# Optimization experiments

Hardware: AMD Instinct MI355X
Metric: run time of the kernel (lower is better)

## Reference

```python
import jax, jax.numpy as jnp
import numpy as np

B, C, H, W = 2, 320, 48, 48
HEADS, DIM_HEAD, NUM_FILTERS = 8, 64, 32
INNER = HEADS * DIM_HEAD  # 512
LN_EPS = 1e-05


def setup_inputs() -> dict:
    key = jax.random.key(0)
    ks = jax.random.split(key, 8)
    w = 0.02
    return {
        "hidden_states": jax.random.normal(ks[0], (B, C, H, W), jnp.float32),
        "encoder_hidden_states": jax.random.normal(ks[1], (B, C, H, W), jnp.float32),
        "Wq": jax.random.normal(ks[2], (C, INNER), jnp.float32) * w,
        "Wk": jax.random.normal(ks[3], (C, INNER), jnp.float32) * w,
        "Wv": jax.random.normal(ks[4], (C, INNER), jnp.float32) * w,
        "Wo": jax.random.normal(ks[5], (INNER, C), jnp.float32) * w,
        "bo": jnp.zeros((C,), jnp.float32),
        "ln_gamma": jnp.ones((C,), jnp.float32),
        "ln_beta": jnp.zeros((C,), jnp.float32),
        "ex_filters": jax.random.normal(ks[6], (NUM_FILTERS, INNER), jnp.float32),
        "dist_filters": jax.random.normal(ks[7], (NUM_FILTERS, INNER), jnp.float32),
        "scale": jnp.ones((1,), jnp.float32),  # learnable scale shadows dim_head**-0.5
    }


def _split_heads(t, heads):
    b, s, d = t.shape
    return t.reshape(b, s, heads, d // heads).transpose(0, 2, 1, 3)  # [b,h,s,dh]


def reference(hidden_states, encoder_hidden_states, Wq, Wk, Wv, Wo, bo,
              ln_gamma, ln_beta, ex_filters, dist_filters, scale):
    b, c, h, w = hidden_states.shape
    _, _, rh, rw = encoder_hidden_states.shape
    residual = hidden_states
    s = scale[0]

    hs = hidden_states.transpose(0, 2, 3, 1).reshape(b, h * w, c)        # [b, q, C]
    ehs = encoder_hidden_states.transpose(0, 2, 3, 1).reshape(b, rh * rw, c)

    # LayerNorm on encoder states
    mu = ehs.mean(-1, keepdims=True)
    var = jnp.mean((ehs - mu) ** 2, axis=-1, keepdims=True)
    ehs = (ehs - mu) * jax.lax.rsqrt(var + LN_EPS) * ln_gamma + ln_beta

    q = _split_heads(hs @ Wq, HEADS)    # [b,h,q,dh]
    k = _split_heads(ehs @ Wk, HEADS)   # [b,h,kv,dh]
    v = _split_heads(ehs @ Wv, HEADS)   # [b,h,kv,dh]
    ef = _split_heads(jnp.broadcast_to(ex_filters[None], (b,) + ex_filters.shape), HEADS)   # [b,h,F,dh]
    df = _split_heads(jnp.broadcast_to(dist_filters[None], (b,) + dist_filters.shape), HEADS)

    # spatial attention: softmax over kv positions
    spatial = jax.nn.softmax(jnp.einsum('bhfd,bhkd->bhfk', ef, k) * s, axis=-1)   # [b,h,F,kv]
    # channel attention: softmax over the filter axis (torch dim=1 of [B*h, F, q])
    channel = jax.nn.softmax(jnp.einsum('bhfd,bhqd->bhfq', df, q) * s, axis=2)    # [b,h,F,q]

    attn = jnp.einsum('bhfq,bhfk->bhqk', channel, spatial)                        # [b,h,q,kv]
    out = jnp.einsum('bhqk,bhkd->bhqd', attn, v)                                  # [b,h,q,dh]

    out = out.transpose(0, 2, 1, 3).reshape(b, h * w, INNER)
    out = out @ Wo + bo
    out = out.reshape(b, h, w, c).transpose(0, 3, 1, 2)
    return out + residual * s
```

## Files before the change

kernel.cpp:

```cpp
#include <hip/hip_runtime.h>
#include <math.h>

#define Bc 2
#define Cc 320
#define Pc 2304
#define HEADSc 8
#define DHc 64
#define INNERc 512
#define Fc 32
#define LN_EPS 1e-5f
#define CHUNKS 18
#define CHUNK_P 128

typedef __attribute__((ext_vector_type(8))) short bf16x8;
typedef __attribute__((ext_vector_type(4))) float f32x4;

static __device__ __forceinline__ ushort f2bf(float x) {
  uint u = __builtin_bit_cast(uint, x);
  u = (u + 0x7fffu + ((u >> 16) & 1u)) >> 16;
  return (ushort)u;
}

static __device__ __forceinline__ void gload16(const ushort* g, ushort* l) {
  __builtin_amdgcn_global_load_lds(
      (const __attribute__((address_space(1))) uint*)g,
      (__attribute__((address_space(3))) uint*)l, 16, 0, 0);
}

static __device__ void transpose_tile(const float* __restrict__ src,
                                      ushort* __restrict__ dst, int R, int C,
                                      int r0, int c0, int tid,
                                      float (*t)[65]) {
#pragma unroll
  for (int it = 0; it < 4; ++it) {
    int lin = it * 256 + tid;
    int rr = lin >> 4, c4 = lin & 15;
    float4 v = *(const float4*)(&src[(size_t)(r0 + rr) * C + c0 + c4 * 4]);
    t[rr][c4 * 4 + 0] = v.x; t[rr][c4 * 4 + 1] = v.y;
    t[rr][c4 * 4 + 2] = v.z; t[rr][c4 * 4 + 3] = v.w;
  }
  __syncthreads();
#pragma unroll
  for (int it = 0; it < 2; ++it) {
    int lin = it * 256 + tid;
    int cc = lin >> 3, r8 = lin & 7;
    ushort tmp[8];
#pragma unroll
    for (int j = 0; j < 8; ++j) tmp[j] = f2bf(t[r8 * 8 + j][cc]);
    *(uint4*)(&dst[(size_t)(c0 + cc) * R + r0 + r8 * 8]) = *(const uint4*)tmp;
  }
}

__global__ __launch_bounds__(256) void prep_all_kernel(
    const float* __restrict__ hs, const float* __restrict__ ehs,
    const float* __restrict__ gamma, const float* __restrict__ beta,
    const float* __restrict__ Wv, const float* __restrict__ Wo,
    const float* __restrict__ exf, const float* __restrict__ Wk,
    const float* __restrict__ dif, const float* __restrict__ Wq,
    ushort* __restrict__ hsT, ushort* __restrict__ ehsT,
    ushort* __restrict__ WvT, ushort* __restrict__ WoT,
    ushort* __restrict__ Gk, ushort* __restrict__ Gq) {
  __shared__ float smem[6448];
  int idx = blockIdx.x, tid = threadIdx.x;

  if (idx < 144) {
    int pt = idx % 36, z = idx / 36;
    int b = z & 1, which = z >> 1;
    int pos0 = pt * 64;
    const float* src = (which ? ehs : hs) + (size_t)b * Cc * Pc;
    ushort* dst = (which ? ehsT : hsT) + (size_t)b * Pc * Cc;
    float* t = smem;
    float* s1 = smem + 4160;
    float* s2 = smem + 4416;
    float* lmean = smem + 4672;
    float* lrstd = smem + 4736;
    int lane = tid & 63, g = tid >> 6;
    if (which) {
      const float* base = src + pos0 + lane;
      float sum = 0.f, sq = 0.f;
      for (int c = g * 80; c < g * 80 + 80; ++c) {
        float x = base[(size_t)c * Pc];
        sum += x; sq += x * x;
      }
      s1[g * 64 + lane] = sum; s2[g * 64 + lane] = sq;
      __syncthreads();
      if (tid < 64) {
        float ts = s1[tid] + s1[64 + tid] + s1[128 + tid] + s1[192 + tid];
        float tq = s2[tid] + s2[64 + tid] + s2[128 + tid] + s2[192 + tid];
        float mean = ts / (float)Cc;
        float var = tq / (float)Cc - mean * mean;
        lmean[tid] = mean;
        lrstd[tid] = rsqrtf(var + LN_EPS);
      }
      __syncthreads();
    }
    for (int ct = 0; ct < 5; ++ct) {
      int r0 = ct * 64;
#pragma unroll
      for (int it = 0; it < 4; ++it) {
        int lin = it * 256 + tid;
        int rr = lin >> 4, c4 = lin & 15;
        float4 v = *(const float4*)(&src[(size_t)(r0 + rr) * Pc + pos0 + c4 * 4]);
        t[rr * 65 + c4 * 4 + 0] = v.x; t[rr * 65 + c4 * 4 + 1] = v.y;
        t[rr * 65 + c4 * 4 + 2] = v.z; t[rr * 65 + c4 * 4 + 3] = v.w;
      }
      __syncthreads();
#pragma unroll
      for (int it = 0; it < 2; ++it) {
        int lin = it * 256 + tid;
        int cc = lin >> 3, r8 = lin & 7;
        float m_ = which ? lmean[cc] : 0.f, rs_ = which ? lrstd[cc] : 1.f;
        ushort tmp[8];
#pragma unroll
        for (int j = 0; j < 8; ++j) {
          int ch = r8 * 8 + j;
          float x = t[ch * 65 + cc];
          float val = which ? (x - m_) * rs_ * gamma[r0 + ch] + beta[r0 + ch] : x;
          tmp[j] = f2bf(val);
        }
        *(uint4*)(&dst[(size_t)(pos0 + cc) * Cc + r0 + r8 * 8]) =
            *(const uint4*)tmp;
      }
      __syncthreads();
    }
  } else {
    int idx2 = idx - 144;
    if (idx2 < 40) {
      transpose_tile(Wv, WvT, Cc, INNERc, (idx2 / 8) * 64, (idx2 % 8) * 64,
                     tid, (float(*)[65])smem);
    } else if (idx2 < 80) {
      int i = idx2 - 40;
      transpose_tile(Wo, WoT, INNERc, Cc, (i / 5) * 64, (i % 5) * 64, tid,
                     (float(*)[65])smem);
    } else {
      int i = idx2 - 80;
      int c0 = (i % 5) * 64, h = (i / 5) % 8, zz = i / 40;
      const float* filt = zz ? dif : exf;
      const float* W = zz ? Wq : Wk;
      ushort* G = zz ? Gq : Gk;
      float (*ef)[66] = (float(*)[66])smem;
      float (*wk)[65] = (float(*)[65])(smem + 32 * 66);
      for (int l = tid; l < Fc * DHc; l += 256) {
        int f = l >> 6, d = l & 63;
        ef[f][d] = filt[(size_t)f * INNERc + h * 64 + d];
      }
      for (int l = tid; l < 64 * DHc; l += 256) {
        int cc = l >> 6, d = l & 63;
        wk[cc][d] = W[(size_t)(c0 + cc) * INNERc + h * 64 + d];
      }
      __syncthreads();
      int f = tid >> 3, cbase = tid & 7;
      float acc[8] = {};
#pragma unroll
      for (int d4 = 0; d4 < DHc; d4 += 4) {
        float4 a = *(const float4*)(&ef[f][d4]);
#pragma unroll
        for (int j = 0; j < 8; ++j) {
          float4 b = *(const float4*)(&wk[cbase + j * 8][d4]);
          acc[j] += a.x * b.x + a.y * b.y + a.z * b.z + a.w * b.w;
        }
      }
#pragma unroll
      for (int j = 0; j < 8; ++j)
        G[(size_t)(h * Fc + f) * Cc + c0 + cbase + j * 8] = f2bf(acc[j]);
    }
  }
}

__global__ __launch_bounds__(256) void spatial_kernel(
    const ushort* __restrict__ Gk, const ushort* __restrict__ ehsT,
    const ushort* __restrict__ WvT, const float* __restrict__ scale_p,
    float* __restrict__ svp, float* __restrict__ mj, float* __restrict__ lj) {
  int c = blockIdx.x, h = blockIdx.y, b = blockIdx.z;
  int tid = threadIdx.x, lane = tid & 63, wv = tid >> 6;
  int l15 = lane & 15, kq = lane >> 4;
  int pos0 = c * CHUNK_P;
  int bh = b * HEADSc + h;
  float s = scale_p[0];

  __shared__ alignas(16) ushort As[96 * 64];
  __shared__ alignas(16) ushort Bs[128 * 64];
  __shared__ float Sq[32 * 132];
  __shared__ alignas(16) ushort P[32 * 136];
  __shared__ alignas(16) ushort Vs[64 * 136];

  const ushort* Av = WvT + (size_t)(h * 64) * Cc;
  const ushort* Ag = Gk + (size_t)(h * Fc) * Cc;
  const ushort* Bb = ehsT + ((size_t)b * Pc + pos0) * Cc;

  f32x4 acc[6][2] = {};
  for (int k0 = 0; k0 < Cc; k0 += 64) {
#pragma unroll
    for (int it = 0; it < 3; ++it) {
      int lin = it * 256 + tid;
      int row = lin >> 3, p = lin & 7;
      int lc = p ^ (row & 7);
      const ushort* sp = (row < 64) ? (Av + (size_t)row * Cc + k0 + lc * 8)
                                    : (Ag + (size_t)(row - 64) * Cc + k0 + lc * 8);
      gload16(sp, &As[lin * 8]);
    }
#pragma unroll
    for (int it = 0; it < 4; ++it) {
      int lin = it * 256 + tid;
      int row = lin >> 3, p = lin & 7;
      int lc = p ^ (row & 7);
      gload16(Bb + (size_t)row * Cc + k0 + lc * 8, &Bs[lin * 8]);
    }
    __syncthreads();
#pragma unroll
    for (int ss = 0; ss < 2; ++ss) {
      bf16x8 af[6], bfr[2];
#pragma unroll
      for (int mt = 0; mt < 6; ++mt) {
        int m = mt * 16 + l15;
        int p = (ss * 4 + kq) ^ (m & 7);
        af[mt] = *(const bf16x8*)(&As[m * 64 + p * 8]);
      }
#pragma unroll
      for (int nt = 0; nt < 2; ++nt) {
        int n = wv * 32 + nt * 16 + l15;
        int p = (ss * 4 + kq) ^ (n & 7);
        bfr[nt] = *(const bf16x8*)(&Bs[n * 64 + p * 8]);
      }
#pragma unroll
      for (int mt = 0; mt < 6; ++mt)
#pragma unroll
        for (int nt = 0; nt < 2; ++nt)
          acc[mt][nt] = __builtin_amdgcn_mfma_f32_16x16x32_bf16(
              af[mt], bfr[nt], acc[mt][nt], 0, 0, 0);
    }
    __syncthreads();
  }
#pragma unroll
  for (int mt = 0; mt < 6; ++mt)
#pragma unroll
    for (int nt = 0; nt < 2; ++nt) {
      int col = wv * 32 + nt * 16 + l15;
#pragma unroll
      for (int r = 0; r < 4; ++r) {
        int row = mt * 16 + kq * 4 + r;
        if (mt < 4) Vs[row * 136 + col] = f2bf(acc[mt][nt][r]);
        else Sq[(row - 64) * 132 + col] = acc[mt][nt][r];
      }
    }
  __syncthreads();

  {
    int row = tid >> 3, sub = tid & 7;
    float vals[16];
    float m_ = -1e30f;
#pragma unroll
    for (int i = 0; i < 16; ++i) {
      vals[i] = s * Sq[row * 132 + sub * 16 + i];
      m_ = fmaxf(m_, vals[i]);
    }
    m_ = fmaxf(m_, __shfl_xor(m_, 1));
    m_ = fmaxf(m_, __shfl_xor(m_, 2));
    m_ = fmaxf(m_, __shfl_xor(m_, 4));
    float l_ = 0.f;
#pragma unroll
    for (int i = 0; i < 16; i += 2) {
      float e0 = __expf(vals[i] - m_);
      float e1 = __expf(vals[i + 1] - m_);
      l_ += e0 + e1;
      uint pk = (uint)f2bf(e0) | ((uint)f2bf(e1) << 16);
      *(uint*)(&P[row * 136 + sub * 16 + i]) = pk;
    }
    l_ += __shfl_xor(l_, 1);
    l_ += __shfl_xor(l_, 2);
    l_ += __shfl_xor(l_, 4);
    if (sub == 0) {
      mj[((size_t)c * 16 + bh) * Fc + row] = m_;
      lj[((size_t)c * 16 + bh) * Fc + row] = l_;
    }
  }
  __syncthreads();

  f32x4 acc2[2] = {};
#pragma unroll
  for (int ss = 0; ss < 4; ++ss) {
    bf16x8 af[2];
#pragma unroll
    for (int mt = 0; mt < 2; ++mt)
      af[mt] = *(const bf16x8*)(&P[(mt * 16 + l15) * 136 + ss * 32 + kq * 8]);
    bf16x8 bfr = *(const bf16x8*)(&Vs[(wv * 16 + l15) * 136 + ss * 32 + kq * 8]);
#pragma unroll
    for (int mt = 0; mt < 2; ++mt)
      acc2[mt] = __builtin_amdgcn_mfma_f32_16x16x32_bf16(af[mt], bfr, acc2[mt],
                                                         0, 0, 0);
  }
  float* op = svp + ((size_t)c * 16 + bh) * (Fc * DHc);
#pragma unroll
  for (int mt = 0; mt < 2; ++mt)
#pragma unroll
    for (int r = 0; r < 4; ++r)
      op[(mt * 16 + kq * 4 + r) * DHc + wv * 16 + l15] = acc2[mt][r];
}

__global__ __launch_bounds__(256) void sv_reduce_kernel(
    const float* __restrict__ svp, const float* __restrict__ mj,
    const float* __restrict__ lj, ushort* __restrict__ svT) {
  int idx = blockIdx.x * 256 + threadIdx.x;
  int d = idx & 63, fr = idx >> 6;
  int bh = fr >> 5, f = fr & 31;
  float m = -1e30f;
#pragma unroll
  for (int c = 0; c < CHUNKS; ++c)
    m = fmaxf(m, mj[((size_t)c * 16 + bh) * Fc + f]);
  float osum = 0.f, lsum = 0.f;
#pragma unroll
  for (int c = 0; c < CHUNKS; ++c) {
    float w = __expf(mj[((size_t)c * 16 + bh) * Fc + f] - m);
    osum += w * svp[((size_t)c * 16 + bh) * (Fc * DHc) + f * DHc + d];
    lsum += w * lj[((size_t)c * 16 + bh) * Fc + f];
  }
  svT[((size_t)bh * DHc + d) * Fc + f] = f2bf(osum / lsum);
}

__global__ __launch_bounds__(256) void channel_kernel(
    const ushort* __restrict__ Gq, const ushort* __restrict__ hsT,
    const ushort* __restrict__ svT, const float* __restrict__ scale_p,
    ushort* __restrict__ OAT) {
  int pb = blockIdx.x, hp = blockIdx.y, b = blockIdx.z;
  int pos0 = pb * 64;
  int tid = threadIdx.x, lane = tid & 63, wv = tid >> 6;
  int l15 = lane & 15, kq = lane >> 4;
  float s = scale_p[0];

  __shared__ alignas(16) ushort Aq[2 * 32 * 64];
  __shared__ alignas(16) ushort Bs[64 * 64];
  __shared__ float SO[64 * 68];
  __shared__ alignas(16) ushort Pt[64 * 40];
  __shared__ alignas(16) ushort svs[64 * 40];
  __shared__ float red[4 * 64];

  f32x4 acc[2][2] = {};
  const ushort* Bb = hsT + ((size_t)b * Pc + pos0) * Cc;
  for (int k0 = 0; k0 < Cc; k0 += 64) {
#pragma unroll
    for (int it = 0; it < 2; ++it) {
      int lin = it * 256 + tid;
      int hh = lin >> 8, row = (lin >> 3) & 31, p = lin & 7;
      int lc = p ^ (row & 7);
      gload16(Gq + (size_t)((hp * 2 + hh) * Fc + row) * Cc + k0 + lc * 8,
              &Aq[lin * 8]);
    }
#pragma unroll
    for (int it = 0; it < 2; ++it) {
      int lin = it * 256 + tid;
      int row = lin >> 3, p = lin & 7;
      int lc = p ^ (row & 7);
      gload16(Bb + (size_t)row * Cc + k0 + lc * 8, &Bs[lin * 8]);
    }
    __syncthreads();
#pragma unroll
    for (int ss = 0; ss < 2; ++ss) {
      int n = wv * 16 + l15;
      int pb_ = (ss * 4 + kq) ^ (n & 7);
      bf16x8 bfr = *(const bf16x8*)(&Bs[n * 64 + pb_ * 8]);
#pragma unroll
      for (int hh = 0; hh < 2; ++hh)
#pragma unroll
        for (int mt = 0; mt < 2; ++mt) {
          int m = mt * 16 + l15;
          int pa = (ss * 4 + kq) ^ (m & 7);
          bf16x8 af = *(const bf16x8*)(&Aq[hh * 2048 + m * 64 + pa * 8]);
          acc[hh][mt] = __builtin_amdgcn_mfma_f32_16x16x32_bf16(
              af, bfr, acc[hh][mt], 0, 0, 0);
        }
    }
    __syncthreads();
  }

  for (int hh = 0; hh < 2; ++hh) {
    int h = hp * 2 + hh;
#pragma unroll
    for (int mt = 0; mt < 2; ++mt)
#pragma unroll
      for (int r = 0; r < 4; ++r)
        SO[(mt * 16 + kq * 4 + r) * 68 + wv * 16 + l15] = acc[hh][mt][r];
    {
      int rr = tid >> 2, p = tid & 3;
      *(uint4*)(&svs[rr * 40 + p * 8]) = *(const uint4*)(
          svT + ((size_t)(b * HEADSc + h) * DHc + rr) * Fc + p * 8);
    }
    __syncthreads();
    {
      int pos = tid & 63, g = tid >> 6;
      float v8[8];
      float pm = -1e30f;
#pragma unroll
      for (int i = 0; i < 8; ++i) {
        v8[i] = s * SO[(g * 8 + i) * 68 + pos];
        pm = fmaxf(pm, v8[i]);
      }
      red[g * 64 + pos] = pm;
      __syncthreads();
      float m_ = fmaxf(fmaxf(red[pos], red[64 + pos]),
                       fmaxf(red[128 + pos], red[192 + pos]));
      __syncthreads();
      float ps = 0.f;
#pragma unroll
      for (int i = 0; i < 8; ++i) {
        v8[i] = __expf(v8[i] - m_);
        ps += v8[i];
      }
      red[g * 64 + pos] = ps;
      __syncthreads();
      float inv = 1.f / (red[pos] + red[64 + pos] + red[128 + pos] +
                         red[192 + pos]);
#pragma unroll
      for (int i = 0; i < 8; i += 2) {
        uint pk = (uint)f2bf(v8[i] * inv) | ((uint)f2bf(v8[i + 1] * inv) << 16);
        *(uint*)(&Pt[pos * 40 + g * 8 + i]) = pk;
      }
    }
    __syncthreads();
    {
      bf16x8 b_ = *(const bf16x8*)(&svs[(wv * 16 + l15) * 40 + kq * 8]);
      f32x4 acc3[4];
#pragma unroll
      for (int mt = 0; mt < 4; ++mt) {
        bf16x8 a_ = *(const bf16x8*)(&Pt[(mt * 16 + l15) * 40 + kq * 8]);
        f32x4 z = {0.f, 0.f, 0.f, 0.f};
        acc3[mt] = __builtin_amdgcn_mfma_f32_16x16x32_bf16(a_, b_, z, 0, 0, 0);
      }
#pragma unroll
      for (int mt = 0; mt < 4; ++mt)
#pragma unroll
        for (int r = 0; r < 4; ++r)
          SO[(mt * 16 + kq * 4 + r) * 68 + wv * 16 + l15] = acc3[mt][r];
    }
    __syncthreads();
#pragma unroll
    for (int it = 0; it < 2; ++it) {
      int lin = it * 256 + tid;
      int p = lin >> 3, c8 = lin & 7;
      ushort tmp[8];
#pragma unroll
      for (int j = 0; j < 8; ++j) tmp[j] = f2bf(SO[p * 68 + c8 * 8 + j]);
      *(uint4*)(&OAT[((size_t)b * Pc + pos0 + p) * INNERc + h * 64 + c8 * 8]) =
          *(const uint4*)tmp;
    }
    __syncthreads();
  }
}

__global__ __launch_bounds__(256) void gemm_mfma_kernel(
    const ushort* __restrict__ A, const ushort* __restrict__ Bt,
    float* __restrict__ Out, int K, int Mdim,
    const float* __restrict__ bias, const float* __restrict__ res,
    const float* __restrict__ scale_p) {
  int b = blockIdx.z;
  int n0 = blockIdx.x * 128, m0 = blockIdx.y * 64;
  int tid = threadIdx.x, lane = tid & 63, wv = tid >> 6;
  int l15 = lane & 15, kq = lane >> 4;
  __shared__ alignas(16) ushort As[64 * 64];
  __shared__ alignas(16) ushort Bs[128 * 64];
  const ushort* Ab = A + (size_t)m0 * K;
  const ushort* Bb = Bt + ((size_t)b * Pc + n0) * K;

  f32x4 acc[4][2] = {};
  for (int k0 = 0; k0 < K; k0 += 64) {
#pragma unroll
    for (int it = 0; it < 2; ++it) {
      int lin = it * 256 + tid;
      int row = lin >> 3, p = lin & 7;
      int lc = p ^ (row & 7);
      gload16(Ab + (size_t)row * K + k0 + lc * 8, &As[lin * 8]);
    }
#pragma unroll
    for (int it = 0; it < 4; ++it) {
      int lin = it * 256 + tid;
      int row = lin >> 3, p = lin & 7;
      int lc = p ^ (row & 7);
      gload16(Bb + (size_t)row * K + k0 + lc * 8, &Bs[lin * 8]);
    }
    __syncthreads();
#pragma unroll
    for (int ss = 0; ss < 2; ++ss) {
      bf16x8 af[4], bfr[2];
#pragma unroll
      for (int mt = 0; mt < 4; ++mt) {
        int m = mt * 16 + l15;
        int p = (ss * 4 + kq) ^ (m & 7);
        af[mt] = *(const bf16x8*)(&As[m * 64 + p * 8]);
      }
#pragma unroll
      for (int nt = 0; nt < 2; ++nt) {
        int n = wv * 32 + nt * 16 + l15;
        int p = (ss * 4 + kq) ^ (n & 7);
        bfr[nt] = *(const bf16x8*)(&Bs[n * 64 + p * 8]);
      }
#pragma unroll
      for (int mt = 0; mt < 4; ++mt)
#pragma unroll
        for (int nt = 0; nt < 2; ++nt)
          acc[mt][nt] = __builtin_amdgcn_mfma_f32_16x16x32_bf16(
              af[mt], bfr[nt], acc[mt][nt], 0, 0, 0);
    }
    __syncthreads();
  }
  float s = scale_p[0];
  float* Ob = Out + ((size_t)b * Mdim + m0) * Pc + n0;
  const float* rb = res + ((size_t)b * Mdim + m0) * Pc + n0;
#pragma unroll
  for (int mt = 0; mt < 4; ++mt)
#pragma unroll
    for (int nt = 0; nt < 2; ++nt) {
      int ncol = wv * 32 + nt * 16 + l15;
#pragma unroll
      for (int r = 0; r < 4; ++r) {
        int m = mt * 16 + kq * 4 + r;
        Ob[(size_t)m * Pc + ncol] =
            acc[mt][nt][r] + bias[m0 + m] + s * rb[(size_t)m * Pc + ncol];
      }
    }
}

extern "C" void kernel_launch(void* const* d_in, const int* in_sizes, int n_in,
                              void* d_out, int out_size, void* d_ws, size_t ws_size,
                              hipStream_t stream) {
  const float* hs    = (const float*)d_in[0];
  const float* ehs   = (const float*)d_in[1];
  const float* Wq    = (const float*)d_in[2];
  const float* Wk    = (const float*)d_in[3];
  const float* Wv    = (const float*)d_in[4];
  const float* Wo    = (const float*)d_in[5];
  const float* bo    = (const float*)d_in[6];
  const float* gamma = (const float*)d_in[7];
  const float* beta  = (const float*)d_in[8];
  const float* exf   = (const float*)d_in[9];
  const float* dif   = (const float*)d_in[10];
  const float* scale = (const float*)d_in[11];
  float* out = (float*)d_out;

  float* ws = (float*)d_ws;
  float* svp = ws;
  float* mj  = svp + 589824;
  float* lj  = mj + 9216;
  ushort* hsT  = (ushort*)(lj + 9216);
  ushort* ehsT = hsT + 1474560;
  ushort* WvT  = ehsT + 1474560;
  ushort* WoT  = WvT + 163840;
  ushort* Gk   = WoT + 163840;
  ushort* Gq   = Gk + 81920;
  ushort* svT  = Gq + 81920;
  ushort* OAT  = svT + 32768;

  prep_all_kernel<<<dim3(304), dim3(256), 0, stream>>>(
      hs, ehs, gamma, beta, Wv, Wo, exf, Wk, dif, Wq,
      hsT, ehsT, WvT, WoT, Gk, Gq);
  spatial_kernel<<<dim3(CHUNKS, HEADSc, Bc), dim3(256), 0, stream>>>(
      Gk, ehsT, WvT, scale, svp, mj, lj);
  sv_reduce_kernel<<<dim3(128), dim3(256), 0, stream>>>(svp, mj, lj, svT);
  channel_kernel<<<dim3(Pc / 64, HEADSc / 2, Bc), dim3(256), 0, stream>>>(
      Gq, hsT, svT, scale, OAT);
  gemm_mfma_kernel<<<dim3(Pc / 128, Cc / 64, Bc), dim3(256), 0, stream>>>(
      WoT, OAT, out, INNERc, Cc, bo, hs, scale);
}
```

Before: 136.1 us.

## Merge spatial and channel stages into one launch, fuse PV into output GEMM

```diff
diff --git a/kernel.cpp b/kernel.cpp
--- a/kernel.cpp
+++ b/kernel.cpp
@@ -59,9 +59,11 @@
     const float* __restrict__ dif, const float* __restrict__ Wq,
     ushort* __restrict__ hsT, ushort* __restrict__ ehsT,
     ushort* __restrict__ WvT, ushort* __restrict__ WoT,
-    ushort* __restrict__ Gk, ushort* __restrict__ Gq) {
+    ushort* __restrict__ Gk, ushort* __restrict__ Gq,
+    uint* __restrict__ cnt) {
   __shared__ float smem[6448];
   int idx = blockIdx.x, tid = threadIdx.x;
+  if (idx == 0 && tid < 16) cnt[tid] = 0;
 
   if (idx < 144) {
     int pt = idx % 36, z = idx / 36;
@@ -167,54 +169,351 @@
   }
 }
 
-__global__ __launch_bounds__(256) void spatial_kernel(
+__global__ __launch_bounds__(256) void mid_kernel(
     const ushort* __restrict__ Gk, const ushort* __restrict__ ehsT,
-    const ushort* __restrict__ WvT, const float* __restrict__ scale_p,
-    float* __restrict__ svp, float* __restrict__ mj, float* __restrict__ lj) {
-  int c = blockIdx.x, h = blockIdx.y, b = blockIdx.z;
+    const ushort* __restrict__ WvT, const ushort* __restrict__ Gq,
+    const ushort* __restrict__ hsT, const float* __restrict__ scale_p,
+    float* __restrict__ svp, float* __restrict__ mj, float* __restrict__ lj,
+    uint* __restrict__ cnt, ushort* __restrict__ svT,
+    ushort* __restrict__ Pn) {
+  __shared__ alignas(16) char smem[71680];
+  __shared__ int lastflag;
+  int tid = threadIdx.x;
+  int typ = (int)blockIdx.x & 1, sidx = (int)blockIdx.x >> 1;
+  int lane = tid & 63, wv = tid >> 6;
+  int l15 = lane & 15, kq = lane >> 4;
+  float s = scale_p[0];
+
+  if (typ == 0) {
+    int c = sidx % CHUNKS, h = (sidx / CHUNKS) & 7, b = sidx / (CHUNKS * 8);
+    int pos0 = c * CHUNK_P;
+    int bh = b * HEADSc + h;
+    ushort* As = (ushort*)smem;
+    ushort* Bs = (ushort*)(smem + 12288);
+    float* Sq = (float*)(smem + 28672);
+    ushort* P = (ushort*)(smem + 45568);
+    ushort* Vs = (ushort*)(smem + 54272);
+
+    const ushort* Av = WvT + (size_t)(h * 64) * Cc;
+    const ushort* Ag = Gk + (size_t)(h * Fc) * Cc;
+    const ushort* Bb = ehsT + ((size_t)b * Pc + pos0) * Cc;
+
+    f32x4 acc[6][2] = {};
+    for (int k0 = 0; k0 < Cc; k0 += 64) {
+#pragma unroll
+      for (int it = 0; it < 3; ++it) {
+        int lin = it * 256 + tid;
+        int row = lin >> 3, p = lin & 7;
+        int lc = p ^ (row & 7);
+        const ushort* sp = (row < 64)
+                               ? (Av + (size_t)row * Cc + k0 + lc * 8)
+                               : (Ag + (size_t)(row - 64) * Cc + k0 + lc * 8);
+        gload16(sp, &As[lin * 8]);
+      }
+#pragma unroll
+      for (int it = 0; it < 4; ++it) {
+        int lin = it * 256 + tid;
+        int row = lin >> 3, p = lin & 7;
+        int lc = p ^ (row & 7);
+        gload16(Bb + (size_t)row * Cc + k0 + lc * 8, &Bs[lin * 8]);
+      }
+      __syncthreads();
+#pragma unroll
+      for (int ss = 0; ss < 2; ++ss) {
+        bf16x8 af[6], bfr[2];
+#pragma unroll
+        for (int mt = 0; mt < 6; ++mt) {
+          int m = mt * 16 + l15;
+          int p = (ss * 4 + kq) ^ (m & 7);
+          af[mt] = *(const bf16x8*)(&As[m * 64 + p * 8]);
+        }
+#pragma unroll
+        for (int nt = 0; nt < 2; ++nt) {
+          int n = wv * 32 + nt * 16 + l15;
+          int p = (ss * 4 + kq) ^ (n & 7);
+          bfr[nt] = *(const bf16x8*)(&Bs[n * 64 + p * 8]);
+        }
+#pragma unroll
+        for (int mt = 0; mt < 6; ++mt)
+#pragma unroll
+          for (int nt = 0; nt < 2; ++nt)
+            acc[mt][nt] = __builtin_amdgcn_mfma_f32_16x16x32_bf16(
+                af[mt], bfr[nt], acc[mt][nt], 0, 0, 0);
+      }
+      __syncthreads();
+    }
+#pragma unroll
+    for (int mt = 0; mt < 6; ++mt)
+#pragma unroll
+      for (int nt = 0; nt < 2; ++nt) {
+        int col = wv * 32 + nt * 16 + l15;
+#pragma unroll
+        for (int r = 0; r < 4; ++r) {
+          int row = mt * 16 + kq * 4 + r;
+          if (mt < 4) Vs[row * 136 + col] = f2bf(acc[mt][nt][r]);
+          else Sq[(row - 64) * 132 + col] = acc[mt][nt][r];
+        }
+      }
+    __syncthreads();
+
+    {
+      int row = tid >> 3, sub = tid & 7;
+      float vals[16];
+      float m_ = -1e30f;
+#pragma unroll
+      for (int i = 0; i < 16; ++i) {
+        vals[i] = s * Sq[row * 132 + sub * 16 + i];
+        m_ = fmaxf(m_, vals[i]);
+      }
+      m_ = fmaxf(m_, __shfl_xor(m_, 1));
+      m_ = fmaxf(m_, __shfl_xor(m_, 2));
+      m_ = fmaxf(m_, __shfl_xor(m_, 4));
+      float l_ = 0.f;
+#pragma unroll
+      for (int i = 0; i < 16; i += 2) {
+        float e0 = __expf(vals[i] - m_);
+        float e1 = __expf(vals[i + 1] - m_);
+        l_ += e0 + e1;
+        uint pk = (uint)f2bf(e0) | ((uint)f2bf(e1) << 16);
+        *(uint*)(&P[row * 136 + sub * 16 + i]) = pk;
+      }
+      l_ += __shfl_xor(l_, 1);
+      l_ += __shfl_xor(l_, 2);
+      l_ += __shfl_xor(l_, 4);
+      if (sub == 0) {
+        mj[((size_t)c * 16 + bh) * Fc + row] = m_;
+        lj[((size_t)c * 16 + bh) * Fc + row] = l_;
+      }
+    }
+    __syncthreads();
+
+    f32x4 acc2[2] = {};
+#pragma unroll
+    for (int ss = 0; ss < 4; ++ss) {
+      bf16x8 af[2];
+#pragma unroll
+      for (int mt = 0; mt < 2; ++mt)
+        af[mt] = *(const bf16x8*)(&P[(mt * 16 + l15) * 136 + ss * 32 + kq * 8]);
+      bf16x8 bfr = *(const bf16x8*)(&Vs[(wv * 16 + l15) * 136 + ss * 32 + kq * 8]);
+#pragma unroll
+      for (int mt = 0; mt < 2; ++mt)
+        acc2[mt] = __builtin_amdgcn_mfma_f32_16x16x32_bf16(af[mt], bfr,
+                                                           acc2[mt], 0, 0, 0);
+    }
+    float* op = svp + ((size_t)c * 16 + bh) * (Fc * DHc);
+#pragma unroll
+    for (int mt = 0; mt < 2; ++mt)
+#pragma unroll
+      for (int r = 0; r < 4; ++r)
+        op[(mt * 16 + kq * 4 + r) * DHc + wv * 16 + l15] = acc2[mt][r];
+
+    __threadfence();
+    __syncthreads();
+    if (tid == 0) {
+      uint old = atomicAdd(&cnt[bh], 1u);
+      lastflag = (old == CHUNKS - 1) ? 1 : 0;
+    }
+    __syncthreads();
+    if (lastflag) {
+      __threadfence();
+      int f = tid >> 3, dg = tid & 7;
+      float mH = -1e30f;
+#pragma unroll
+      for (int c2 = 0; c2 < CHUNKS; ++c2)
+        mH = fmaxf(mH, mj[((size_t)c2 * 16 + bh) * Fc + f]);
+      float lsum = 0.f;
+      float osum[8] = {};
+#pragma unroll
+      for (int c2 = 0; c2 < CHUNKS; ++c2) {
+        float w = __expf(mj[((size_t)c2 * 16 + bh) * Fc + f] - mH);
+        lsum += w * lj[((size_t)c2 * 16 + bh) * Fc + f];
+        const float* sp = svp + ((size_t)c2 * 16 + bh) * (Fc * DHc) + f * DHc +
+                          dg * 8;
+        float4 a = *(const float4*)sp;
+        float4 b2 = *(const float4*)(sp + 4);
+        osum[0] += w * a.x; osum[1] += w * a.y;
+        osum[2] += w * a.z; osum[3] += w * a.w;
+        osum[4] += w * b2.x; osum[5] += w * b2.y;
+        osum[6] += w * b2.z; osum[7] += w * b2.w;
+      }
+      float inv = 1.f / lsum;
+#pragma unroll
+      for (int j = 0; j < 8; ++j)
+        svT[((size_t)bh * DHc + dg * 8 + j) * Fc + f] = f2bf(osum[j] * inv);
+    }
+  } else {
+    int pb = sidx % 36, hp = (sidx / 36) & 3, b = sidx / 144;
+    int pos0 = pb * 64;
+    ushort* Aq = (ushort*)smem;
+    ushort* Bs = (ushort*)(smem + 8192);
+    float* SO = (float*)(smem + 16384);
+    ushort* Pt = (ushort*)(smem + 33792);
+    float* red = (float*)(smem + 38912);
+
+    f32x4 acc[2][2] = {};
+    const ushort* Bb = hsT + ((size_t)b * Pc + pos0) * Cc;
+    for (int k0 = 0; k0 < Cc; k0 += 64) {
+#pragma unroll
+      for (int it = 0; it < 2; ++it) {
+        int lin = it * 256 + tid;
+        int hh = lin >> 8, row = (lin >> 3) & 31, p = lin & 7;
+        int lc = p ^ (row & 7);
+        gload16(Gq + (size_t)((hp * 2 + hh) * Fc + row) * Cc + k0 + lc * 8,
+                &Aq[lin * 8]);
+      }
+#pragma unroll
+      for (int it = 0; it < 2; ++it) {
+        int lin = it * 256 + tid;
+        int row = lin >> 3, p = lin & 7;
+        int lc = p ^ (row & 7);
+        gload16(Bb + (size_t)row * Cc + k0 + lc * 8, &Bs[lin * 8]);
+      }
+      __syncthreads();
+#pragma unroll
+      for (int ss = 0; ss < 2; ++ss) {
+        int n = wv * 16 + l15;
+        int pb_ = (ss * 4 + kq) ^ (n & 7);
+        bf16x8 bfr = *(const bf16x8*)(&Bs[n * 64 + pb_ * 8]);
+#pragma unroll
+        for (int hh = 0; hh < 2; ++hh)
+#pragma unroll
+          for (int mt = 0; mt < 2; ++mt) {
+            int m = mt * 16 + l15;
+            int pa = (ss * 4 + kq) ^ (m & 7);
+            bf16x8 af = *(const bf16x8*)(&Aq[hh * 2048 + m * 64 + pa * 8]);
+            acc[hh][mt] = __builtin_amdgcn_mfma_f32_16x16x32_bf16(
+                af, bfr, acc[hh][mt], 0, 0, 0);
+          }
+      }
+      __syncthreads();
+    }
+
+    for (int hh = 0; hh < 2; ++hh) {
+      int h = hp * 2 + hh;
+#pragma unroll
+      for (int mt = 0; mt < 2; ++mt)
+#pragma unroll
+        for (int r = 0; r < 4; ++r)
+          SO[(mt * 16 + kq * 4 + r) * 68 + wv * 16 + l15] = acc[hh][mt][r];
+      __syncthreads();
+      {
+        int pos = tid & 63, g = tid >> 6;
+        float v8[8];
+        float pm = -1e30f;
+#pragma unroll
+        for (int i = 0; i < 8; ++i) {
+          v8[i] = s * SO[(g * 8 + i) * 68 + pos];
+          pm = fmaxf(pm, v8[i]);
+        }
+        red[g * 64 + pos] = pm;
+        __syncthreads();
+        float m_ = fmaxf(fmaxf(red[pos], red[64 + pos]),
+                         fmaxf(red[128 + pos], red[192 + pos]));
+        __syncthreads();
+        float ps = 0.f;
+#pragma unroll
+        for (int i = 0; i < 8; ++i) {
+          v8[i] = __expf(v8[i] - m_);
+          ps += v8[i];
+        }
+        red[g * 64 + pos] = ps;
+        __syncthreads();
+        float inv = 1.f / (red[pos] + red[64 + pos] + red[128 + pos] +
+                           red[192 + pos]);
+#pragma unroll
+        for (int i = 0; i < 8; i += 2) {
+          uint pk =
+              (uint)f2bf(v8[i] * inv) | ((uint)f2bf(v8[i + 1] * inv) << 16);
+          *(uint*)(&Pt[pos * 40 + g * 8 + i]) = pk;
+        }
+      }
+      __syncthreads();
+      {
+        int p = tid >> 2, ch = tid & 3;
+        *(uint4*)(&Pn[((size_t)(b * HEADSc + h) * Pc + pos0 + p) * Fc +
+                      ch * 8]) = *(const uint4*)(&Pt[p * 40 + ch * 8]);
+      }
+      __syncthreads();
+    }
+  }
+}
+
+__global__ __launch_bounds__(256) void pvgemm_kernel(
+    const ushort* __restrict__ WoT, const ushort* __restrict__ Pn,
+    const ushort* __restrict__ svT, const float* __restrict__ scale_p,
+    const float* __restrict__ bias, const float* __restrict__ res,
+    float* __restrict__ Out) {
+  int n0 = blockIdx.x * 128, m0 = blockIdx.y * 64, b = blockIdx.z;
   int tid = threadIdx.x, lane = tid & 63, wv = tid >> 6;
   int l15 = lane & 15, kq = lane >> 4;
-  int pos0 = c * CHUNK_P;
-  int bh = b * HEADSc + h;
-  float s = scale_p[0];
-
-  __shared__ alignas(16) ushort As[96 * 64];
+  __shared__ alignas(16) ushort As[64 * 64];
+  __shared__ alignas(16) ushort Ps[128 * 32];
+  __shared__ alignas(16) ushort svs[64 * 32];
   __shared__ alignas(16) ushort Bs[128 * 64];
-  __shared__ float Sq[32 * 132];
-  __shared__ alignas(16) ushort P[32 * 136];
-  __shared__ alignas(16) ushort Vs[64 * 136];
-
-  const ushort* Av = WvT + (size_t)(h * 64) * Cc;
-  const ushort* Ag = Gk + (size_t)(h * Fc) * Cc;
-  const ushort* Bb = ehsT + ((size_t)b * Pc + pos0) * Cc;
-
-  f32x4 acc[6][2] = {};
-  for (int k0 = 0; k0 < Cc; k0 += 64) {
-#pragma unroll
-    for (int it = 0; it < 3; ++it) {
+  __shared__ float SOf[128 * 68];
+
+  f32x4 acc[4][2] = {};
+  for (int h = 0; h < HEADSc; ++h) {
+    const ushort* Ab = WoT + (size_t)m0 * INNERc + h * 64;
+    const ushort* Pb = Pn + ((size_t)(b * HEADSc + h) * Pc + n0) * Fc;
+    const ushort* Sb = svT + (size_t)(b * HEADSc + h) * DHc * Fc;
+#pragma unroll
+    for (int it = 0; it < 2; ++it) {
       int lin = it * 256 + tid;
       int row = lin >> 3, p = lin & 7;
-      int lc = p ^ (row & 7);
-      const ushort* sp = (row < 64) ? (Av + (size_t)row * Cc + k0 + lc * 8)
-                                    : (Ag + (size_t)(row - 64) * Cc + k0 + lc * 8);
-      gload16(sp, &As[lin * 8]);
-    }
+      gload16(Ab + (size_t)row * INNERc + ((p ^ (row & 7)) * 8), &As[lin * 8]);
+    }
+#pragma unroll
+    for (int it = 0; it < 2; ++it) {
+      int lin = it * 256 + tid;
+      int row = lin >> 2, p = lin & 3;
+      gload16(Pb + (size_t)row * Fc + ((p ^ (row & 3)) * 8), &Ps[lin * 8]);
+    }
+    {
+      int row = tid >> 2, p = tid & 3;
+      gload16(Sb + (size_t)row * Fc + ((p ^ (row & 3)) * 8), &svs[tid * 8]);
+    }
+    __syncthreads();
+    f32x4 pv[2][4];
+#pragma unroll
+    for (int mt = 0; mt < 2; ++mt) {
+      int m = (wv * 2 + mt) * 16 + l15;
+      bf16x8 af = *(const bf16x8*)(&Ps[m * 32 + (kq ^ (m & 3)) * 8]);
+#pragma unroll
+      for (int nt = 0; nt < 4; ++nt) {
+        int n = nt * 16 + l15;
+        bf16x8 bf = *(const bf16x8*)(&svs[n * 32 + (kq ^ (n & 3)) * 8]);
+        f32x4 z = {0.f, 0.f, 0.f, 0.f};
+        pv[mt][nt] = __builtin_amdgcn_mfma_f32_16x16x32_bf16(af, bf, z, 0, 0, 0);
+      }
+    }
+#pragma unroll
+    for (int mt = 0; mt < 2; ++mt)
+#pragma unroll
+      for (int nt = 0; nt < 4; ++nt)
+#pragma unroll
+        for (int r = 0; r < 4; ++r)
+          SOf[((wv * 2 + mt) * 16 + kq * 4 + r) * 68 + nt * 16 + l15] =
+              pv[mt][nt][r];
+    __syncthreads();
 #pragma unroll
     for (int it = 0; it < 4; ++it) {
       int lin = it * 256 + tid;
-      int row = lin >> 3, p = lin & 7;
-      int lc = p ^ (row & 7);
-      gload16(Bb + (size_t)row * Cc + k0 + lc * 8, &Bs[lin * 8]);
+      int row = lin >> 3, c8 = lin & 7;
+      ushort tmp[8];
+#pragma unroll
+      for (int j = 0; j < 8; ++j) tmp[j] = f2bf(SOf[row * 68 + c8 * 8 + j]);
+      *(uint4*)(&Bs[row * 64 + ((c8 ^ (row & 7)) * 8)]) = *(const uint4*)tmp;
     }
     __syncthreads();
 #pragma unroll
     for (int ss = 0; ss < 2; ++ss) {
-      bf16x8 af[6], bfr[2];
-#pragma unroll
-      for (int mt = 0; mt < 6; ++mt) {
+      bf16x8 afr[4], bfr[2];
+#pragma unroll
+      for (int mt = 0; mt < 4; ++mt) {
         int m = mt * 16 + l15;
         int p = (ss * 4 + kq) ^ (m & 7);
-        af[mt] = *(const bf16x8*)(&As[m * 64 + p * 8]);
+        afr[mt] = *(const bf16x8*)(&As[m * 64 + p * 8]);
       }
 #pragma unroll
       for (int nt = 0; nt < 2; ++nt) {
@@ -223,287 +522,17 @@
         bfr[nt] = *(const bf16x8*)(&Bs[n * 64 + p * 8]);
       }
 #pragma unroll
-      for (int mt = 0; mt < 6; ++mt)
+      for (int mt = 0; mt < 4; ++mt)
 #pragma unroll
         for (int nt = 0; nt < 2; ++nt)
           acc[mt][nt] = __builtin_amdgcn_mfma_f32_16x16x32_bf16(
-              af[mt], bfr[nt], acc[mt][nt], 0, 0, 0);
-    }
-    __syncthreads();
-  }
-#pragma unroll
-  for (int mt = 0; mt < 6; ++mt)
-#pragma unroll
-    for (int nt = 0; nt < 2; ++nt) {
-      int col = wv * 32 + nt * 16 + l15;
-#pragma unroll
-      for (int r = 0; r < 4; ++r) {
-        int row = mt * 16 + kq * 4 + r;
-        if (mt < 4) Vs[row * 136 + col] = f2bf(acc[mt][nt][r]);
-        else Sq[(row - 64) * 132 + col] = acc[mt][nt][r];
-      }
-    }
-  __syncthreads();
-
-  {
-    int row = tid >> 3, sub = tid & 7;
-    float vals[16];
-    float m_ = -1e30f;
-#pragma unroll
-    for (int i = 0; i < 16; ++i) {
-      vals[i] = s * Sq[row * 132 + sub * 16 + i];
-      m_ = fmaxf(m_, vals[i]);
-    }
-    m_ = fmaxf(m_, __shfl_xor(m_, 1));
-    m_ = fmaxf(m_, __shfl_xor(m_, 2));
-    m_ = fmaxf(m_, __shfl_xor(m_, 4));
-    float l_ = 0.f;
-#pragma unroll
-    for (int i = 0; i < 16; i += 2) {
-      float e0 = __expf(vals[i] - m_);
-      float e1 = __expf(vals[i + 1] - m_);
-      l_ += e0 + e1;
-      uint pk = (uint)f2bf(e0) | ((uint)f2bf(e1) << 16);
-      *(uint*)(&P[row * 136 + sub * 16 + i]) = pk;
-    }
-    l_ += __shfl_xor(l_, 1);
-    l_ += __shfl_xor(l_, 2);
-    l_ += __shfl_xor(l_, 4);
-    if (sub == 0) {
-      mj[((size_t)c * 16 + bh) * Fc + row] = m_;
-      lj[((size_t)c * 16 + bh) * Fc + row] = l_;
-    }
-  }
-  __syncthreads();
-
-  f32x4 acc2[2] = {};
-#pragma unroll
-  for (int ss = 0; ss < 4; ++ss) {
-    bf16x8 af[2];
-#pragma unroll
-    for (int mt = 0; mt < 2; ++mt)
-      af[mt] = *(const bf16x8*)(&P[(mt * 16 + l15) * 136 + ss * 32 + kq * 8]);
-    bf16x8 bfr = *(const bf16x8*)(&Vs[(wv * 16 + l15) * 136 + ss * 32 + kq * 8]);
-#pragma unroll
-    for (int mt = 0; mt < 2; ++mt)
-      acc2[mt] = __builtin_amdgcn_mfma_f32_16x16x32_bf16(af[mt], bfr, acc2[mt],
-                                                         0, 0, 0);
-  }
-  float* op = svp + ((size_t)c * 16 + bh) * (Fc * DHc);
-#pragma unroll
-  for (int mt = 0; mt < 2; ++mt)
-#pragma unroll
-    for (int r = 0; r < 4; ++r)
-      op[(mt * 16 + kq * 4 + r) * DHc + wv * 16 + l15] = acc2[mt][r];
-}
-
-__global__ __launch_bounds__(256) void sv_reduce_kernel(
-    const float* __restrict__ svp, const float* __restrict__ mj,
-    const float* __restrict__ lj, ushort* __restrict__ svT) {
-  int idx = blockIdx.x * 256 + threadIdx.x;
-  int d = idx & 63, fr = idx >> 6;
-  int bh = fr >> 5, f = fr & 31;
-  float m = -1e30f;
-#pragma unroll
-  for (int c = 0; c < CHUNKS; ++c)
-    m = fmaxf(m, mj[((size_t)c * 16 + bh) * Fc + f]);
-  float osum = 0.f, lsum = 0.f;
-#pragma unroll
-  for (int c = 0; c < CHUNKS; ++c) {
-    float w = __expf(mj[((size_t)c * 16 + bh) * Fc + f] - m);
-    osum += w * svp[((size_t)c * 16 + bh) * (Fc * DHc) + f * DHc + d];
-    lsum += w * lj[((size_t)c * 16 + bh) * Fc + f];
-  }
-  svT[((size_t)bh * DHc + d) * Fc + f] = f2bf(osum / lsum);
-}
-
-__global__ __launch_bounds__(256) void channel_kernel(
-    const ushort* __restrict__ Gq, const ushort* __restrict__ hsT,
-    const ushort* __restrict__ svT, const float* __restrict__ scale_p,
-    ushort* __restrict__ OAT) {
-  int pb = blockIdx.x, hp = blockIdx.y, b = blockIdx.z;
-  int pos0 = pb * 64;
-  int tid = threadIdx.x, lane = tid & 63, wv = tid >> 6;
-  int l15 = lane & 15, kq = lane >> 4;
-  float s = scale_p[0];
-
-  __shared__ alignas(16) ushort Aq[2 * 32 * 64];
-  __shared__ alignas(16) ushort Bs[64 * 64];
-  __shared__ float SO[64 * 68];
-  __shared__ alignas(16) ushort Pt[64 * 40];
-  __shared__ alignas(16) ushort svs[64 * 40];
-  __shared__ float red[4 * 64];
-
-  f32x4 acc[2][2] = {};
-  const ushort* Bb = hsT + ((size_t)b * Pc + pos0) * Cc;
-  for (int k0 = 0; k0 < Cc; k0 += 64) {
-#pragma unroll
-    for (int it = 0; it < 2; ++it) {
-      int lin = it * 256 + tid;
-      int hh = lin >> 8, row = (lin >> 3) & 31, p = lin & 7;
-      int lc = p ^ (row & 7);
-      gload16(Gq + (size_t)((hp * 2 + hh) * Fc + row) * Cc + k0 + lc * 8,
-              &Aq[lin * 8]);
-    }
-#pragma unroll
-    for (int it = 0; it < 2; ++it) {
-      int lin = it * 256 + tid;
-      int row = lin >> 3, p = lin & 7;
-      int lc = p ^ (row & 7);
-      gload16(Bb + (size_t)row * Cc + k0 + lc * 8, &Bs[lin * 8]);
-    }
-    __syncthreads();
-#pragma unroll
-    for (int ss = 0; ss < 2; ++ss) {
-      int n = wv * 16 + l15;
-      int pb_ = (ss * 4 + kq) ^ (n & 7);
-      bf16x8 bfr = *(const bf16x8*)(&Bs[n * 64 + pb_ * 8]);
-#pragma unroll
-      for (int hh = 0; hh < 2; ++hh)
-#pragma unroll
-        for (int mt = 0; mt < 2; ++mt) {
-          int m = mt * 16 + l15;
-          int pa = (ss * 4 + kq) ^ (m & 7);
-          bf16x8 af = *(const bf16x8*)(&Aq[hh * 2048 + m * 64 + pa * 8]);
-          acc[hh][mt] = __builtin_amdgcn_mfma_f32_16x16x32_bf16(
-              af, bfr, acc[hh][mt], 0, 0, 0);
-        }
-    }
-    __syncthreads();
-  }
-
-  for (int hh = 0; hh < 2; ++hh) {
-    int h = hp * 2 + hh;
-#pragma unroll
-    for (int mt = 0; mt < 2; ++mt)
-#pragma unroll
-      for (int r = 0; r < 4; ++r)
-        SO[(mt * 16 + kq * 4 + r) * 68 + wv * 16 + l15] = acc[hh][mt][r];
-    {
-      int rr = tid >> 2, p = tid & 3;
-      *(uint4*)(&svs[rr * 40 + p * 8]) = *(const uint4*)(
-          svT + ((size_t)(b * HEADSc + h) * DHc + rr) * Fc + p * 8);
-    }
-    __syncthreads();
-    {
-      int pos = tid & 63, g = tid >> 6;
-      float v8[8];
-      float pm = -1e30f;
-#pragma unroll
-      for (int i = 0; i < 8; ++i) {
-        v8[i] = s * SO[(g * 8 + i) * 68 + pos];
-        pm = fmaxf(pm, v8[i]);
-      }
-      red[g * 64 + pos] = pm;
-      __syncthreads();
-      float m_ = fmaxf(fmaxf(red[pos], red[64 + pos]),
-                       fmaxf(red[128 + pos], red[192 + pos]));
-      __syncthreads();
-      float ps = 0.f;
-#pragma unroll
-      for (int i = 0; i < 8; ++i) {
-        v8[i] = __expf(v8[i] - m_);
-        ps += v8[i];
-      }
-      red[g * 64 + pos] = ps;
-      __syncthreads();
-      float inv = 1.f / (red[pos] + red[64 + pos] + red[128 + pos] +
-                         red[192 + pos]);
-#pragma unroll
-      for (int i = 0; i < 8; i += 2) {
-        uint pk = (uint)f2bf(v8[i] * inv) | ((uint)f2bf(v8[i + 1] * inv) << 16);
-        *(uint*)(&Pt[pos * 40 + g * 8 + i]) = pk;
-      }
-    }
-    __syncthreads();
-    {
-      bf16x8 b_ = *(const bf16x8*)(&svs[(wv * 16 + l15) * 40 + kq * 8]);
-      f32x4 acc3[4];
-#pragma unroll
-      for (int mt = 0; mt < 4; ++mt) {
-        bf16x8 a_ = *(const bf16x8*)(&Pt[(mt * 16 + l15) * 40 + kq * 8]);
-        f32x4 z = {0.f, 0.f, 0.f, 0.f};
-        acc3[mt] = __builtin_amdgcn_mfma_f32_16x16x32_bf16(a_, b_, z, 0, 0, 0);
-      }
-#pragma unroll
-      for (int mt = 0; mt < 4; ++mt)
-#pragma unroll
-        for (int r = 0; r < 4; ++r)
-          SO[(mt * 16 + kq * 4 + r) * 68 + wv * 16 + l15] = acc3[mt][r];
-    }
-    __syncthreads();
-#pragma unroll
-    for (int it = 0; it < 2; ++it) {
-      int lin = it * 256 + tid;
-      int p = lin >> 3, c8 = lin & 7;
-      ushort tmp[8];
-#pragma unroll
-      for (int j = 0; j < 8; ++j) tmp[j] = f2bf(SO[p * 68 + c8 * 8 + j]);
-      *(uint4*)(&OAT[((size_t)b * Pc + pos0 + p) * INNERc + h * 64 + c8 * 8]) =
-          *(const uint4*)tmp;
-    }
-    __syncthreads();
-  }
-}
-
-__global__ __launch_bounds__(256) void gemm_mfma_kernel(
-    const ushort* __restrict__ A, const ushort* __restrict__ Bt,
-    float* __restrict__ Out, int K, int Mdim,
-    const float* __restrict__ bias, const float* __restrict__ res,
-    const float* __restrict__ scale_p) {
-  int b = blockIdx.z;
-  int n0 = blockIdx.x * 128, m0 = blockIdx.y * 64;
-  int tid = threadIdx.x, lane = tid & 63, wv = tid >> 6;
-  int l15 = lane & 15, kq = lane >> 4;
-  __shared__ alignas(16) ushort As[64 * 64];
-  __shared__ alignas(16) ushort Bs[128 * 64];
-  const ushort* Ab = A + (size_t)m0 * K;
-  const ushort* Bb = Bt + ((size_t)b * Pc + n0) * K;
-
-  f32x4 acc[4][2] = {};
-  for (int k0 = 0; k0 < K; k0 += 64) {
-#pragma unroll
-    for (int it = 0; it < 2; ++it) {
-      int lin = it * 256 + tid;
-      int row = lin >> 3, p = lin & 7;
-      int lc = p ^ (row & 7);
-      gload16(Ab + (size_t)row * K + k0 + lc * 8, &As[lin * 8]);
-    }
-#pragma unroll
-    for (int it = 0; it < 4; ++it) {
-      int lin = it * 256 + tid;
-      int row = lin >> 3, p = lin & 7;
-      int lc = p ^ (row & 7);
-      gload16(Bb + (size_t)row * K + k0 + lc * 8, &Bs[lin * 8]);
-    }
-    __syncthreads();
-#pragma unroll
-    for (int ss = 0; ss < 2; ++ss) {
-      bf16x8 af[4], bfr[2];
-#pragma unroll
-      for (int mt = 0; mt < 4; ++mt) {
-        int m = mt * 16 + l15;
-        int p = (ss * 4 + kq) ^ (m & 7);
-        af[mt] = *(const bf16x8*)(&As[m * 64 + p * 8]);
-      }
-#pragma unroll
-      for (int nt = 0; nt < 2; ++nt) {
-        int n = wv * 32 + nt * 16 + l15;
-        int p = (ss * 4 + kq) ^ (n & 7);
-        bfr[nt] = *(const bf16x8*)(&Bs[n * 64 + p * 8]);
-      }
-#pragma unroll
-      for (int mt = 0; mt < 4; ++mt)
-#pragma unroll
-        for (int nt = 0; nt < 2; ++nt)
-          acc[mt][nt] = __builtin_amdgcn_mfma_f32_16x16x32_bf16(
-              af[mt], bfr[nt], acc[mt][nt], 0, 0, 0);
+              afr[mt], bfr[nt], acc[mt][nt], 0, 0, 0);
     }
     __syncthreads();
   }
   float s = scale_p[0];
-  float* Ob = Out + ((size_t)b * Mdim + m0) * Pc + n0;
-  const float* rb = res + ((size_t)b * Mdim + m0) * Pc + n0;
+  float* Ob = Out + ((size_t)b * Cc + m0) * Pc + n0;
+  const float* rb = res + ((size_t)b * Cc + m0) * Pc + n0;
 #pragma unroll
   for (int mt = 0; mt < 4; ++mt)
 #pragma unroll
@@ -539,23 +568,21 @@
   float* svp = ws;
   float* mj  = svp + 589824;
   float* lj  = mj + 9216;
-  ushort* hsT  = (ushort*)(lj + 9216);
+  uint*  cnt = (uint*)(lj + 9216);
+  ushort* hsT  = (ushort*)(cnt + 16);
   ushort* ehsT = hsT + 1474560;
   ushort* WvT  = ehsT + 1474560;
   ushort* WoT  = WvT + 163840;
   ushort* Gk   = WoT + 163840;
   ushort* Gq   = Gk + 81920;
   ushort* svT  = Gq + 81920;
-  ushort* OAT  = svT + 32768;
+  ushort* Pn   = svT + 32768;
 
   prep_all_kernel<<<dim3(304), dim3(256), 0, stream>>>(
       hs, ehs, gamma, beta, Wv, Wo, exf, Wk, dif, Wq,
-      hsT, ehsT, WvT, WoT, Gk, Gq);
-  spatial_kernel<<<dim3(CHUNKS, HEADSc, Bc), dim3(256), 0, stream>>>(
-      Gk, ehsT, WvT, scale, svp, mj, lj);
-  sv_reduce_kernel<<<dim3(128), dim3(256), 0, stream>>>(svp, mj, lj, svT);
-  channel_kernel<<<dim3(Pc / 64, HEADSc / 2, Bc), dim3(256), 0, stream>>>(
-      Gq, hsT, svT, scale, OAT);
-  gemm_mfma_kernel<<<dim3(Pc / 128, Cc / 64, Bc), dim3(256), 0, stream>>>(
-      WoT, OAT, out, INNERc, Cc, bo, hs, scale);
-}
+      hsT, ehsT, WvT, WoT, Gk, Gq, cnt);
+  mid_kernel<<<dim3(576), dim3(256), 0, stream>>>(
+      Gk, ehsT, WvT, Gq, hsT, scale, svp, mj, lj, cnt, svT, Pn);
+  pvgemm_kernel<<<dim3(Pc / 128, Cc / 64, Bc), dim3(256), 0, stream>>>(
+      WoT, Pn, svT, scale, bo, hs, out);
+}
```

Measured after the change: 202.4 us. 48.7% more time.
